# Performance work log

Measured on AMD Instinct MI355X. Metric: run time of the kernel, lower is better.

## Reference

```python
import jax, jax.numpy as jnp
import numpy as np

MAX_FRAMES = 12
TOPK = 49
NUM_SAMPLES = 256
SIGMA = 0.05
LN_EPS = 1e-5


def setup_inputs() -> dict:
    key = jax.random.key(0)
    ks = jax.random.split(key, 6)
    B, MF, N, D = 8, MAX_FRAMES, 197, 512
    x = jax.random.normal(ks[0], (B, MF * N, D), dtype=jnp.float32)
    noise = jax.random.normal(ks[1], (B * MF, NUM_SAMPLES, N - 1), dtype=jnp.float32)
    ln_gamma = jnp.ones((D,), jnp.float32)
    ln_beta = jnp.zeros((D,), jnp.float32)
    w_in = jax.random.normal(ks[2], (D, D // 2), dtype=jnp.float32) * 0.02
    w1 = jax.random.normal(ks[3], (D, D // 2), dtype=jnp.float32) * 0.02
    w2 = jax.random.normal(ks[4], (D // 2, 1), dtype=jnp.float32) * 0.02
    return {"x": x, "noise": noise, "ln_gamma": ln_gamma, "ln_beta": ln_beta,
            "w_in": w_in, "w1": w1, "w2": w2}


def reference(x, noise, ln_gamma, ln_beta, w_in, w1, w2):
    B, L, D = x.shape
    N = L // MAX_FRAMES
    xf = x.reshape(B * MAX_FRAMES, N, D)          # (b, N, D)

    # PredictorLG: LayerNorm -> Linear -> GELU (torch GELU is exact erf)
    mu = xf.mean(-1, keepdims=True)
    var = xf.var(-1, keepdims=True)               # biased, matches torch LayerNorm
    hn = (xf - mu) * jax.lax.rsqrt(var + LN_EPS) * ln_gamma + ln_beta
    h = jax.nn.gelu(hn @ w_in, approximate=False)  # (b, N, D/2)
    # concat local features with broadcast global (cls-token) features
    g = jnp.broadcast_to(h[:, :1, :], h.shape)
    cat = jnp.concatenate([h, g], axis=-1)         # (b, N, D)
    score = jnp.tanh(jax.nn.gelu(cat @ w1, approximate=False) @ w2)[..., 0]  # (b, N)

    sp = score[:, 1:]                              # (b, d) spatial scores, d = N-1
    b_eff, ns, d = noise.shape
    pert = sp[:, None, :] + noise * SIGMA          # (b, ns, d)

    # top-k set per sample; sorted ascending (matches torch sort of topk indices)
    order = jnp.argsort(-pert, axis=-1)            # descending by value
    top_sorted = jnp.sort(order[..., :TOPK], axis=-1)  # (b, ns, k)

    # mean of one-hots == scatter-add counts / num_samples (avoids one-hot blowup)
    bi = jnp.arange(b_eff)[:, None, None]
    pos = jnp.arange(TOPK)[None, None, :]
    ind = jnp.zeros((b_eff, TOPK, d), x.dtype).at[bi, pos, top_sorted].add(1.0) / ns

    cls_feat = xf[:, :1, :]                        # (b, 1, D)
    spat_feat = xf[:, 1:, :]                       # (b, d, D)
    sel = jnp.einsum('bkl,bld->bkd', ind, spat_feat)  # (b, k, D)
    out = jnp.concatenate([cls_feat, sel], axis=1)    # (b, 1+k, D)
    return out.reshape(B, MAX_FRAMES * (1 + TOPK), D)
```

## Files before the change

kernel.cpp:

```cpp
#include <hip/hip_runtime.h>
#include <math.h>

#define NFRAME 96
#define NTOK   197
#define NSPAT  196
#define DIM    512
#define DH     256
#define NSAMP  256
#define KSEL   49
#define SIG    0.05f
#define MPAD   208
#define MTOT   (NFRAME * MPAD)

typedef unsigned short u16;
typedef __attribute__((ext_vector_type(8))) short bf16x8;
typedef __attribute__((ext_vector_type(4))) float f32x4;

__device__ __forceinline__ float gelu_exact(float v) {
    return 0.5f * v * (1.0f + erff(v * 0.70710678118654752440f));
}
__device__ __forceinline__ unsigned bf16_rne(float f) {
    unsigned u = __float_as_uint(f);
    return (u + 0x7fffu + ((u >> 16) & 1u)) >> 16;
}
__device__ __forceinline__ float bf16_to_f(unsigned h) {
    return __uint_as_float(h << 16);
}

__global__ __launch_bounds__(256) void k0_prep(
    const float* __restrict__ x, const float* __restrict__ gamma,
    const float* __restrict__ beta,
    const float* __restrict__ w_in, const float* __restrict__ w1,
    u16* __restrict__ wiT_hi, u16* __restrict__ wiT_lo,
    u16* __restrict__ w1T_hi, u16* __restrict__ w1T_lo,
    u16* __restrict__ xs_hi, u16* __restrict__ xs_lo)
{
    if (blockIdx.x < 512) {
        const int n = blockIdx.x & 255, which = blockIdx.x >> 8;
        const float* w = which ? w1 : w_in;
        u16* th = which ? w1T_hi : wiT_hi;
        u16* tl = which ? w1T_lo : wiT_lo;
        for (int k = threadIdx.x; k < DIM; k += 256) {
            float v = w[(size_t)k * DH + n];
            unsigned hi = bf16_rne(v);
            unsigned lo = bf16_rne(v - bf16_to_f(hi));
            th[(size_t)n * DIM + k] = (u16)hi;
            tl[(size_t)n * DIM + k] = (u16)lo;
        }
        return;
    }
    const int row  = (blockIdx.x - 512) * 4 + (threadIdx.x >> 6);
    const int lane = threadIdx.x & 63;
    const int f = row / MPAD;
    int rr = row - f * MPAD; if (rr > NTOK - 1) rr = NTOK - 1;
    const float* xr = x + ((size_t)f * NTOK + rr) * DIM + lane * 8;
    float4 a = *(const float4*)xr, b4 = *(const float4*)(xr + 4);
    float e[8] = {a.x, a.y, a.z, a.w, b4.x, b4.y, b4.z, b4.w};
    float s = 0.f, sq = 0.f;
    #pragma unroll
    for (int j = 0; j < 8; ++j) { s += e[j]; sq += e[j] * e[j]; }
    #pragma unroll
    for (int o = 32; o > 0; o >>= 1) {
        s  += __shfl_xor(s,  o, 64);
        sq += __shfl_xor(sq, o, 64);
    }
    const float mu  = s * (1.f / 512.f);
    const float var = sq * (1.f / 512.f) - mu * mu;
    const float rs  = 1.f / sqrtf(var + 1e-5f);

    const float* gp = gamma + lane * 8;
    const float* bp = beta + lane * 8;
    float4 g0 = *(const float4*)gp, g1 = *(const float4*)(gp + 4);
    float4 b0 = *(const float4*)bp, b1 = *(const float4*)(bp + 4);
    float gg[8] = {g0.x, g0.y, g0.z, g0.w, g1.x, g1.y, g1.z, g1.w};
    float bt[8] = {b0.x, b0.y, b0.z, b0.w, b1.x, b1.y, b1.z, b1.w};

    unsigned hw[4], lw[4];
    #pragma unroll
    for (int p = 0; p < 4; ++p) {
        float s0 = rs * gg[2*p],   s1 = rs * gg[2*p+1];
        float v0 = e[2*p]   * s0 + (bt[2*p]   - mu * s0);
        float v1 = e[2*p+1] * s1 + (bt[2*p+1] - mu * s1);
        unsigned h0 = bf16_rne(v0), h1 = bf16_rne(v1);
        float l0 = v0 - bf16_to_f(h0), l1 = v1 - bf16_to_f(h1);
        hw[p] = h0 | (h1 << 16);
        lw[p] = bf16_rne(l0) | (bf16_rne(l1) << 16);
    }
    size_t off = (size_t)row * DIM + lane * 8;
    *(uint4*)(xs_hi + off) = make_uint4(hw[0], hw[1], hw[2], hw[3]);
    *(uint4*)(xs_lo + off) = make_uint4(lw[0], lw[1], lw[2], lw[3]);
}

#define LDG 72
__global__ __launch_bounds__(256, 2) void k1_gemm1(
    const u16* __restrict__ xs_hi, const u16* __restrict__ xs_lo,
    const u16* __restrict__ wiT_hi, const u16* __restrict__ wiT_lo,
    u16* __restrict__ h_hi, u16* __restrict__ h_lo)
{
    __shared__ u16 Ah[2][64][LDG], Al[2][64][LDG], Bh[2][64][LDG], Bl[2][64][LDG];
    const int t = threadIdx.x, lane = t & 63, wv = t >> 6;
    const int linear = (blockIdx.x & 7) * 156 + (blockIdx.x >> 3);
    const int Mb = linear >> 2, Nb = linear & 3;
    const int R0 = Mb * 64, N0 = Nb * 64;
    const int wm = wv >> 1, wn = wv & 1;
    const int m15 = lane & 15, q = lane >> 4;

    f32x4 acc[2][2];
    #pragma unroll
    for (int i = 0; i < 2; ++i)
        #pragma unroll
        for (int j = 0; j < 2; ++j)
            acc[i][j] = (f32x4){0.f, 0.f, 0.f, 0.f};

    const int ar = t >> 2, as = (t & 3) * 16;
    const size_t abase = (size_t)(R0 + ar) * DIM + as;
    const size_t bbase = (size_t)(N0 + ar) * DIM + as;

    uint4 pAh0 = *(const uint4*)(xs_hi + abase);
    uint4 pAh1 = *(const uint4*)(xs_hi + abase + 8);
    uint4 pAl0 = *(const uint4*)(xs_lo + abase);
    uint4 pAl1 = *(const uint4*)(xs_lo + abase + 8);
    uint4 pBh0 = *(const uint4*)(wiT_hi + bbase);
    uint4 pBh1 = *(const uint4*)(wiT_hi + bbase + 8);
    uint4 pBl0 = *(const uint4*)(wiT_lo + bbase);
    uint4 pBl1 = *(const uint4*)(wiT_lo + bbase + 8);

    for (int k0 = 0; k0 < DIM; k0 += 64) {
        const int p = (k0 >> 6) & 1;
        *(uint4*)&Ah[p][ar][as]     = pAh0;
        *(uint4*)&Ah[p][ar][as + 8] = pAh1;
        *(uint4*)&Al[p][ar][as]     = pAl0;
        *(uint4*)&Al[p][ar][as + 8] = pAl1;
        *(uint4*)&Bh[p][ar][as]     = pBh0;
        *(uint4*)&Bh[p][ar][as + 8] = pBh1;
        *(uint4*)&Bl[p][ar][as]     = pBl0;
        *(uint4*)&Bl[p][ar][as + 8] = pBl1;
        if (k0 + 64 < DIM) {
            pAh0 = *(const uint4*)(xs_hi + abase + k0 + 64);
            pAh1 = *(const uint4*)(xs_hi + abase + k0 + 72);
            pAl0 = *(const uint4*)(xs_lo + abase + k0 + 64);
            pAl1 = *(const uint4*)(xs_lo + abase + k0 + 72);
            pBh0 = *(const uint4*)(wiT_hi + bbase + k0 + 64);
            pBh1 = *(const uint4*)(wiT_hi + bbase + k0 + 72);
            pBl0 = *(const uint4*)(wiT_lo + bbase + k0 + 64);
            pBl1 = *(const uint4*)(wiT_lo + bbase + k0 + 72);
        }
        __syncthreads();

        #pragma unroll
        for (int kh = 0; kh < 2; ++kh) {
            const int ko = kh * 32 + q * 8;
            bf16x8 ah[2], al[2], bh[2], bl[2];
            #pragma unroll
            for (int i = 0; i < 2; ++i) {
                ah[i] = *(const bf16x8*)&Ah[p][wm*32 + i*16 + m15][ko];
                al[i] = *(const bf16x8*)&Al[p][wm*32 + i*16 + m15][ko];
                bh[i] = *(const bf16x8*)&Bh[p][wn*32 + i*16 + m15][ko];
                bl[i] = *(const bf16x8*)&Bl[p][wn*32 + i*16 + m15][ko];
            }
            #pragma unroll
            for (int mt = 0; mt < 2; ++mt)
                #pragma unroll
                for (int nt = 0; nt < 2; ++nt) {
                    f32x4 c = acc[mt][nt];
                    c = __builtin_amdgcn_mfma_f32_16x16x32_bf16(ah[mt], bh[nt], c, 0, 0, 0);
                    c = __builtin_amdgcn_mfma_f32_16x16x32_bf16(al[mt], bh[nt], c, 0, 0, 0);
                    c = __builtin_amdgcn_mfma_f32_16x16x32_bf16(ah[mt], bl[nt], c, 0, 0, 0);
                    acc[mt][nt] = c;
                }
        }
    }

    #pragma unroll
    for (int mt = 0; mt < 2; ++mt)
        #pragma unroll
        for (int nt = 0; nt < 2; ++nt)
            #pragma unroll
            for (int reg = 0; reg < 4; ++reg) {
                int r = R0 + wm*32 + mt*16 + q*4 + reg;
                int c = N0 + wn*32 + nt*16 + m15;
                float v = gelu_exact(acc[mt][nt][reg]);
                unsigned hb = bf16_rne(v);
                unsigned lb = bf16_rne(v - bf16_to_f(hb));
                size_t off = (size_t)r * DH + c;
                h_hi[off] = (u16)hb;
                h_lo[off] = (u16)lb;
            }
}

__global__ __launch_bounds__(256, 2) void k1_gemm2(
    const u16* __restrict__ h_hi, const u16* __restrict__ h_lo,
    const u16* __restrict__ w1T_hi, const u16* __restrict__ w1T_lo,
    const float* __restrict__ w2, float* __restrict__ s_quar)
{
    __shared__ u16 Ah[2][64][LDG], Al[2][64][LDG], Bh[2][64][LDG], Bl[2][64][LDG];
    __shared__ float red[2][2][32];
    const int t = threadIdx.x, lane = t & 63, wv = t >> 6;
    const int linear = (blockIdx.x & 7) * 156 + (blockIdx.x >> 3);
    const int Mb = linear >> 2, Nb = linear & 3;
    const int R0 = Mb * 64, N0 = Nb * 64;
    const int wm = wv >> 1, wn = wv & 1;
    const int m15 = lane & 15, q = lane >> 4;

    f32x4 acc[2][2];
    #pragma unroll
    for (int i = 0; i < 2; ++i)
        #pragma unroll
        for (int j = 0; j < 2; ++j)
            acc[i][j] = (f32x4){0.f, 0.f, 0.f, 0.f};

    const int ar = t >> 2, as = (t & 3) * 16;
    const int agrow = R0 + ar;
    const size_t arow_off = (size_t)agrow * DH;
    const size_t g0_off   = (size_t)((agrow / MPAD) * MPAD) * DH;
    const size_t bbase = (size_t)(N0 + ar) * DIM + as;

    auto asrc = [&](int k0) -> size_t {
        return (k0 < DH) ? (arow_off + k0 + as) : (g0_off + (k0 - DH) + as);
    };

    uint4 pAh0 = *(const uint4*)(h_hi + asrc(0));
    uint4 pAh1 = *(const uint4*)(h_hi + asrc(0) + 8);
    uint4 pAl0 = *(const uint4*)(h_lo + asrc(0));
    uint4 pAl1 = *(const uint4*)(h_lo + asrc(0) + 8);
    uint4 pBh0 = *(const uint4*)(w1T_hi + bbase);
    uint4 pBh1 = *(const uint4*)(w1T_hi + bbase + 8);
    uint4 pBl0 = *(const uint4*)(w1T_lo + bbase);
    uint4 pBl1 = *(const uint4*)(w1T_lo + bbase + 8);

    for (int k0 = 0; k0 < DIM; k0 += 64) {
        const int p = (k0 >> 6) & 1;
        *(uint4*)&Ah[p][ar][as]     = pAh0;
        *(uint4*)&Ah[p][ar][as + 8] = pAh1;
        *(uint4*)&Al[p][ar][as]     = pAl0;
        *(uint4*)&Al[p][ar][as + 8] = pAl1;
        *(uint4*)&Bh[p][ar][as]     = pBh0;
        *(uint4*)&Bh[p][ar][as + 8] = pBh1;
        *(uint4*)&Bl[p][ar][as]     = pBl0;
        *(uint4*)&Bl[p][ar][as + 8] = pBl1;
        if (k0 + 64 < DIM) {
            size_t srcn = asrc(k0 + 64);
            pAh0 = *(const uint4*)(h_hi + srcn);
            pAh1 = *(const uint4*)(h_hi + srcn + 8);
            pAl0 = *(const uint4*)(h_lo + srcn);
            pAl1 = *(const uint4*)(h_lo + srcn + 8);
            pBh0 = *(const uint4*)(w1T_hi + bbase + k0 + 64);
            pBh1 = *(const uint4*)(w1T_hi + bbase + k0 + 72);
            pBl0 = *(const uint4*)(w1T_lo + bbase + k0 + 64);
            pBl1 = *(const uint4*)(w1T_lo + bbase + k0 + 72);
        }
        __syncthreads();

        #pragma unroll
        for (int kh = 0; kh < 2; ++kh) {
            const int ko = kh * 32 + q * 8;
            bf16x8 ah[2], al[2], bh[2], bl[2];
            #pragma unroll
            for (int i = 0; i < 2; ++i) {
                ah[i] = *(const bf16x8*)&Ah[p][wm*32 + i*16 + m15][ko];
                al[i] = *(const bf16x8*)&Al[p][wm*32 + i*16 + m15][ko];
                bh[i] = *(const bf16x8*)&Bh[p][wn*32 + i*16 + m15][ko];
                bl[i] = *(const bf16x8*)&Bl[p][wn*32 + i*16 + m15][ko];
            }
            #pragma unroll
            for (int mt = 0; mt < 2; ++mt)
                #pragma unroll
                for (int nt = 0; nt < 2; ++nt) {
                    f32x4 c = acc[mt][nt];
                    c = __builtin_amdgcn_mfma_f32_16x16x32_bf16(ah[mt], bh[nt], c, 0, 0, 0);
                    c = __builtin_amdgcn_mfma_f32_16x16x32_bf16(al[mt], bh[nt], c, 0, 0, 0);
                    c = __builtin_amdgcn_mfma_f32_16x16x32_bf16(ah[mt], bl[nt], c, 0, 0, 0);
                    acc[mt][nt] = c;
                }
        }
    }

    float w2v[2];
    #pragma unroll
    for (int nt = 0; nt < 2; ++nt) w2v[nt] = w2[N0 + wn*32 + nt*16 + m15];
    #pragma unroll
    for (int mt = 0; mt < 2; ++mt)
        #pragma unroll
        for (int reg = 0; reg < 4; ++reg) {
            float s = gelu_exact(acc[mt][0][reg]) * w2v[0] +
                      gelu_exact(acc[mt][1][reg]) * w2v[1];
            #pragma unroll
            for (int o = 1; o <= 8; o <<= 1)
                s += __shfl_xor(s, o, 64);
            if (m15 == 0)
                red[wn][wm][mt*16 + q*4 + reg] = s;
        }
    __syncthreads();
    if (t < 64) {
        int wmj = t >> 5, rl = t & 31;
        float sv = red[0][wmj][rl] + red[1][wmj][rl];
        s_quar[(size_t)Nb * MTOT + R0 + t] = sv;
    }
}

__global__ __launch_bounds__(1024) void k2_select(
    const float* __restrict__ s_quar, const float* __restrict__ noise,
    int* __restrict__ hist2)
{
    const int fb   = blockIdx.x;
    const int f    = fb >> 1;
    const int half = fb & 1;
    const int t    = threadIdx.x;
    const int lane = t & 63;
    const int wv   = t >> 6;

    __shared__ int hist_s[KSEL * NSPAT];
    for (int i = t; i < KSEL * NSPAT; i += 1024) hist_s[i] = 0;

    const float* s0 = s_quar;
    const float* s1 = s_quar + MTOT;
    const float* s2 = s_quar + 2 * (size_t)MTOT;
    const float* s3 = s_quar + 3 * (size_t)MTOT;
    float spv[4];
    #pragma unroll
    for (int j = 0; j < 4; ++j) {
        int l = lane + 64 * j;
        if (l < NSPAT) {
            size_t idx = (size_t)f * MPAD + 1 + l;
            spv[j] = tanhf(s0[idx] + s1[idx] + s2[idx] + s3[idx]);
        } else spv[j] = 0.f;
    }
    __syncthreads();

    const unsigned long long lmask = (1ull << lane) - 1ull;

    for (int si = 0; si < 8; ++si) {
        const int s = half * 128 + wv * 8 + si;
        const float* nz = noise + ((size_t)f * NSAMP + s) * NSPAT;
        unsigned key[4];
        #pragma unroll
        for (int j = 0; j < 4; ++j) {
            int l = lane + 64 * j;
            if (l < NSPAT) {
                float p = spv[j] + nz[l] * SIG;
                unsigned u = __float_as_uint(p);
                key[j] = (u & 0x80000000u) ? ~u : (u | 0x80000000u);
            } else {
                key[j] = 0u;
            }
        }

        unsigned ans;
        {
            int c31 = 0;
            #pragma unroll
            for (int j = 0; j < 4; ++j)
                c31 += __popcll(__ballot(key[j] >= 0x80000000u));
            ans = (c31 >= KSEL) ? 0x80000000u : 0x40000000u;
        }
        for (int bit = 29; bit >= 0; --bit) {
            unsigned cand = ans | (1u << bit);
            int cnt = 0;
            #pragma unroll
            for (int j = 0; j < 4; ++j)
                cnt += __popcll(__ballot(key[j] >= cand));
            if (cnt >= KSEL) ans = cand;
        }

        unsigned long long eq[4];
        int cgt = 0;
        #pragma unroll
        for (int j = 0; j < 4; ++j) {
            cgt += __popcll(__ballot(key[j] > ans));
            eq[j] = __ballot(key[j] == ans);
        }
        const int quota = KSEL - cgt;
        int eqpre[4]; { int run = 0;
            #pragma unroll
            for (int j = 0; j < 4; ++j) { eqpre[j] = run; run += __popcll(eq[j]); } }

        int pre = 0;
        #pragma unroll
        for (int j = 0; j < 4; ++j) {
            bool iseq = (key[j] == ans);
            int trk = eqpre[j] + __popcll(eq[j] & lmask);
            bool selj = (key[j] > ans) || (iseq && trk < quota);
            unsigned long long sb = __ballot(selj);
            int rk = pre + __popcll(sb & lmask);
            if (selj)
                atomicAdd(&hist_s[rk * NSPAT + lane + 64 * j], 1);
            pre += __popcll(sb);
        }
    }

    __syncthreads();
    int* hb = hist2 + (size_t)fb * (KSEL * NSPAT);
    for (int i = t; i < KSEL * NSPAT; i += 1024)
        hb[i] = hist_s[i];
}

#define KP3 52
__global__ __launch_bounds__(256) void k3_output(
    const float* __restrict__ x, const int* __restrict__ hist2,
    float* __restrict__ out)
{
    const int b   = blockIdx.x >> 3;
    const int ds  = blockIdx.x & 7;
    const int d0  = ds * 64;
    const int t   = threadIdx.x;
    const int tdc = t & 15;
    const int tk  = t >> 4;

    __shared__ float hist_s[NSPAT * KP3 + 16];

    const int* h0 = hist2 + (size_t)(2 * b) * (KSEL * NSPAT);
    const int* h1 = h0 + KSEL * NSPAT;
    for (int i = t; i < KSEL * NSPAT; i += 256) {
        int k = i / NSPAT;
        int l = i - k * NSPAT;
        hist_s[l * KP3 + k] = (float)(h0[i] + h1[i]);
    }
    for (int i = t; i < NSPAT * 3 + 16; i += 256) {
        int l = i / 3, j = i - l * 3;
        int idx = (i < NSPAT * 3) ? (l * KP3 + KSEL + j) : (NSPAT * KP3 + i - NSPAT * 3);
        hist_s[idx] = 0.f;
    }
    if (t < 64)
        out[(size_t)b * 50 * DIM + d0 + t] = x[(size_t)b * NTOK * DIM + d0 + t];
    __syncthreads();

    const float* xs = x + ((size_t)b * NTOK + 1) * DIM + d0 + tdc * 4;
    float4 acc[4];
    #pragma unroll
    for (int i = 0; i < 4; ++i) acc[i] = make_float4(0.f, 0.f, 0.f, 0.f);

    #pragma unroll 7
    for (int l = 0; l < NSPAT; ++l) {
        float4 v  = *(const float4*)(xs + (size_t)l * DIM);
        float4 w4 = *(const float4*)&hist_s[l * KP3 + tk * 4];
        acc[0].x += w4.x * v.x; acc[0].y += w4.x * v.y;
        acc[0].z += w4.x * v.z; acc[0].w += w4.x * v.w;
        acc[1].x += w4.y * v.x; acc[1].y += w4.y * v.y;
        acc[1].z += w4.y * v.z; acc[1].w += w4.y * v.w;
        acc[2].x += w4.z * v.x; acc[2].y += w4.z * v.y;
        acc[2].z += w4.z * v.z; acc[2].w += w4.z * v.w;
        acc[3].x += w4.w * v.x; acc[3].y += w4.w * v.y;
        acc[3].z += w4.w * v.z; acc[3].w += w4.w * v.w;
    }

    const float inv = 1.f / 256.f;
    #pragma unroll
    for (int i = 0; i < 4; ++i) {
        int k = tk * 4 + i;
        if (k < KSEL) {
            float4 o = make_float4(acc[i].x * inv, acc[i].y * inv,
                                   acc[i].z * inv, acc[i].w * inv);
            *(float4*)&out[((size_t)b * 50 + 1 + k) * DIM + d0 + tdc * 4] = o;
        }
    }
}

extern "C" void kernel_launch(void* const* d_in, const int* in_sizes, int n_in,
                              void* d_out, int out_size, void* d_ws, size_t ws_size,
                              hipStream_t stream)
{
    const float* x     = (const float*)d_in[0];
    const float* noise = (const float*)d_in[1];
    const float* gamma = (const float*)d_in[2];
    const float* beta  = (const float*)d_in[3];
    const float* w_in  = (const float*)d_in[4];
    const float* w1    = (const float*)d_in[5];
    const float* w2    = (const float*)d_in[6];
    float* out = (float*)d_out;

    char* ws = (char*)d_ws;
    int*   hist2   = (int*)  (ws + 0);
    float* s_quar  = (float*)(ws + 7375872);
    u16*   wiT_hi  = (u16*)  (ws + 7695360);
    u16*   wiT_lo  = (u16*)  (ws + 7957504);
    u16*   w1T_hi  = (u16*)  (ws + 8219648);
    u16*   w1T_lo  = (u16*)  (ws + 8481792);
    u16*   h_hi    = (u16*)  (ws + 8743936);
    u16*   h_lo    = (u16*)  (ws + 18967552);
    u16*   xs_hi   = (u16*)  (ws + 29191168);
    u16*   xs_lo   = (u16*)  (ws + 49638400);

    k0_prep<<<512 + MTOT / 4, 256, 0, stream>>>(x, gamma, beta, w_in, w1,
                                                wiT_hi, wiT_lo, w1T_hi, w1T_lo,
                                                xs_hi, xs_lo);
    k1_gemm1<<<(MTOT / 64) * 4, 256, 0, stream>>>(xs_hi, xs_lo, wiT_hi, wiT_lo,
                                                  h_hi, h_lo);
    k1_gemm2<<<(MTOT / 64) * 4, 256, 0, stream>>>(h_hi, h_lo, w1T_hi, w1T_lo,
                                                  w2, s_quar);
    k2_select<<<NFRAME * 2, 1024, 0, stream>>>(s_quar, noise, hist2);
    k3_output<<<NFRAME * 8, 256, 0, stream>>>(x, hist2, out);
}
```

Before: 217.0 us.

## Precompute per-frame global-feature bias to halve gemm2 K dimension

The global (cls-token) half of the concatenated input is identical for every row of a frame, so its product with the second half of w1 is computed once per frame in a new small kernel and added as a bias. The main gemm2 loop then runs over K=256 instead of 512, removing half of its MFMA work and loads. In exchange it adds an extra kernel launch and per-element gbias loads in the epilogue. gbias shares workspace with hist2, which is only safe if hist2 is written after gemm2 consumes gbias.

```diff
diff --git a/kernel.cpp b/kernel.cpp
--- a/kernel.cpp
+++ b/kernel.cpp
@@ -188,10 +188,41 @@
             }
 }
 
+__global__ __launch_bounds__(256) void k1g_gbias(
+    const u16* __restrict__ h_hi, const u16* __restrict__ h_lo,
+    const u16* __restrict__ w1T_hi, const u16* __restrict__ w1T_lo,
+    float* __restrict__ gbias)
+{
+    const int f = blockIdx.x, n = threadIdx.x;
+    const size_t hoff = (size_t)f * MPAD * DH;
+    const size_t woff = (size_t)n * DIM + DH;
+    float s = 0.f;
+    for (int k = 0; k < DH; k += 8) {
+        uint4 vh = *(const uint4*)(h_hi + hoff + k);
+        uint4 vl = *(const uint4*)(h_lo + hoff + k);
+        uint4 uh = *(const uint4*)(w1T_hi + woff + k);
+        uint4 ul = *(const uint4*)(w1T_lo + woff + k);
+        const unsigned* ph = (const unsigned*)&vh;
+        const unsigned* pl = (const unsigned*)&vl;
+        const unsigned* qh = (const unsigned*)&uh;
+        const unsigned* ql = (const unsigned*)&ul;
+        #pragma unroll
+        for (int w = 0; w < 4; ++w) {
+            float a0 = bf16_to_f(ph[w] & 0xffffu) + bf16_to_f(pl[w] & 0xffffu);
+            float a1 = bf16_to_f(ph[w] >> 16)     + bf16_to_f(pl[w] >> 16);
+            float b0 = bf16_to_f(qh[w] & 0xffffu) + bf16_to_f(ql[w] & 0xffffu);
+            float b1 = bf16_to_f(qh[w] >> 16)     + bf16_to_f(ql[w] >> 16);
+            s += a0 * b0 + a1 * b1;
+        }
+    }
+    gbias[f * DH + n] = s;
+}
+
 __global__ __launch_bounds__(256, 2) void k1_gemm2(
     const u16* __restrict__ h_hi, const u16* __restrict__ h_lo,
     const u16* __restrict__ w1T_hi, const u16* __restrict__ w1T_lo,
-    const float* __restrict__ w2, float* __restrict__ s_quar)
+    const float* __restrict__ w2, const float* __restrict__ gbias,
+    float* __restrict__ s_quar)
 {
     __shared__ u16 Ah[2][64][LDG], Al[2][64][LDG], Bh[2][64][LDG], Bl[2][64][LDG];
     __shared__ float red[2][2][32];
@@ -210,25 +241,19 @@
             acc[i][j] = (f32x4){0.f, 0.f, 0.f, 0.f};
 
     const int ar = t >> 2, as = (t & 3) * 16;
-    const int agrow = R0 + ar;
-    const size_t arow_off = (size_t)agrow * DH;
-    const size_t g0_off   = (size_t)((agrow / MPAD) * MPAD) * DH;
+    const size_t abase = (size_t)(R0 + ar) * DH + as;
     const size_t bbase = (size_t)(N0 + ar) * DIM + as;
 
-    auto asrc = [&](int k0) -> size_t {
-        return (k0 < DH) ? (arow_off + k0 + as) : (g0_off + (k0 - DH) + as);
-    };
-
-    uint4 pAh0 = *(const uint4*)(h_hi + asrc(0));
-    uint4 pAh1 = *(const uint4*)(h_hi + asrc(0) + 8);
-    uint4 pAl0 = *(const uint4*)(h_lo + asrc(0));
-    uint4 pAl1 = *(const uint4*)(h_lo + asrc(0) + 8);
+    uint4 pAh0 = *(const uint4*)(h_hi + abase);
+    uint4 pAh1 = *(const uint4*)(h_hi + abase + 8);
+    uint4 pAl0 = *(const uint4*)(h_lo + abase);
+    uint4 pAl1 = *(const uint4*)(h_lo + abase + 8);
     uint4 pBh0 = *(const uint4*)(w1T_hi + bbase);
     uint4 pBh1 = *(const uint4*)(w1T_hi + bbase + 8);
     uint4 pBl0 = *(const uint4*)(w1T_lo + bbase);
     uint4 pBl1 = *(const uint4*)(w1T_lo + bbase + 8);
 
-    for (int k0 = 0; k0 < DIM; k0 += 64) {
+    for (int k0 = 0; k0 < DH; k0 += 64) {
         const int p = (k0 >> 6) & 1;
         *(uint4*)&Ah[p][ar][as]     = pAh0;
         *(uint4*)&Ah[p][ar][as + 8] = pAh1;
@@ -238,12 +263,11 @@
         *(uint4*)&Bh[p][ar][as + 8] = pBh1;
         *(uint4*)&Bl[p][ar][as]     = pBl0;
         *(uint4*)&Bl[p][ar][as + 8] = pBl1;
-        if (k0 + 64 < DIM) {
-            size_t srcn = asrc(k0 + 64);
-            pAh0 = *(const uint4*)(h_hi + srcn);
-            pAh1 = *(const uint4*)(h_hi + srcn + 8);
-            pAl0 = *(const uint4*)(h_lo + srcn);
-            pAl1 = *(const uint4*)(h_lo + srcn + 8);
+        if (k0 + 64 < DH) {
+            pAh0 = *(const uint4*)(h_hi + abase + k0 + 64);
+            pAh1 = *(const uint4*)(h_hi + abase + k0 + 72);
+            pAl0 = *(const uint4*)(h_lo + abase + k0 + 64);
+            pAl1 = *(const uint4*)(h_lo + abase + k0 + 72);
             pBh0 = *(const uint4*)(w1T_hi + bbase + k0 + 64);
             pBh1 = *(const uint4*)(w1T_hi + bbase + k0 + 72);
             pBl0 = *(const uint4*)(w1T_lo + bbase + k0 + 64);
@@ -276,14 +300,22 @@
     }
 
     float w2v[2];
-    #pragma unroll
-    for (int nt = 0; nt < 2; ++nt) w2v[nt] = w2[N0 + wn*32 + nt*16 + m15];
+    int   cIdx[2];
+    #pragma unroll
+    for (int nt = 0; nt < 2; ++nt) {
+        cIdx[nt] = N0 + wn*32 + nt*16 + m15;
+        w2v[nt]  = w2[cIdx[nt]];
+    }
     #pragma unroll
     for (int mt = 0; mt < 2; ++mt)
         #pragma unroll
         for (int reg = 0; reg < 4; ++reg) {
-            float s = gelu_exact(acc[mt][0][reg]) * w2v[0] +
-                      gelu_exact(acc[mt][1][reg]) * w2v[1];
+            int r = R0 + wm*32 + mt*16 + q*4 + reg;
+            int f = r / MPAD;
+            float gb0 = gbias[f * DH + cIdx[0]];
+            float gb1 = gbias[f * DH + cIdx[1]];
+            float s = gelu_exact(acc[mt][0][reg] + gb0) * w2v[0] +
+                      gelu_exact(acc[mt][1][reg] + gb1) * w2v[1];
             #pragma unroll
             for (int o = 1; o <= 8; o <<= 1)
                 s += __shfl_xor(s, o, 64);
@@ -470,6 +502,7 @@
 
     char* ws = (char*)d_ws;
     int*   hist2   = (int*)  (ws + 0);
+    float* gbias   = (float*)(ws + 0);
     float* s_quar  = (float*)(ws + 7375872);
     u16*   wiT_hi  = (u16*)  (ws + 7695360);
     u16*   wiT_lo  = (u16*)  (ws + 7957504);
@@ -485,8 +518,9 @@
                                                 xs_hi, xs_lo);
     k1_gemm1<<<(MTOT / 64) * 4, 256, 0, stream>>>(xs_hi, xs_lo, wiT_hi, wiT_lo,
                                                   h_hi, h_lo);
+    k1g_gbias<<<NFRAME, 256, 0, stream>>>(h_hi, h_lo, w1T_hi, w1T_lo, gbias);
     k1_gemm2<<<(MTOT / 64) * 4, 256, 0, stream>>>(h_hi, h_lo, w1T_hi, w1T_lo,
-                                                  w2, s_quar);
+                                                  w2, gbias, s_quar);
     k2_select<<<NFRAME * 2, 1024, 0, stream>>>(s_quar, noise, hist2);
     k3_output<<<NFRAME * 8, 256, 0, stream>>>(x, hist2, out);
 }
```

Result: no change. 221.4 us (+2.0%).
